# Kernel optimization log

Hardware: AMD Instinct MI355X
Metric: run time of the kernel (lower is better)

Reference implementation:

```python
import jax, jax.numpy as jnp
import numpy as np

TOP_K = 2  # matches init_kwargs top_k


def setup_inputs() -> dict:
    key = jax.random.key(0)
    ks = jax.random.split(key, 7)
    d_model, d_ff, E = 512, 2048, 8
    B, S = 2, 2048
    std = 0.02
    return {
        "x": jax.random.normal(ks[0], (B, S, d_model), dtype=jnp.float32),
        "Wr": jax.random.normal(ks[1], (E, d_model), dtype=jnp.float32) * std,
        "br": jnp.zeros((E,), dtype=jnp.float32),
        "W1": jax.random.normal(ks[2], (E, d_model, d_ff), dtype=jnp.float32) * (1.0 / np.sqrt(d_model)),
        "b1": jnp.zeros((E, d_ff), dtype=jnp.float32),
        "W2": jax.random.normal(ks[3], (E, d_ff, d_model), dtype=jnp.float32) * (1.0 / np.sqrt(d_ff)),
        "b2": jnp.zeros((E, d_model), dtype=jnp.float32),
    }


def _moe_forward(x, Wr, br, W1, b1, W2, b2):
    leading = x.shape[:-1]
    d = x.shape[-1]
    E = Wr.shape[0]
    xf = x.reshape(-1, d)                                   # [N, d]
    N = xf.shape[0]

    # --- token router (linear head) ---
    logits = xf @ Wr.T + br                                  # [N, E]
    routing = jax.nn.softmax(logits, axis=-1)                # [N, E]
    sel_w, sel_idx = jax.lax.top_k(routing, TOP_K)           # [N, K]
    sel_w = sel_w / jnp.sum(sel_w, axis=-1, keepdims=True)   # renormalize top-k

    # combine weights as dense [N, E] (zero for unselected experts)
    combine = jnp.zeros((N, E), dtype=xf.dtype).at[
        jnp.arange(N)[:, None], sel_idx
    ].add(sel_w)                                             # [N, E]

    # --- expert FFNs (dense all-expert compute, masked combine) ---
    h = jax.nn.gelu(jnp.einsum("nd,edf->enf", xf, W1) + b1[:, None, :])  # [E, N, ff]
    y = jnp.einsum("enf,efd->end", h, W2) + b2[:, None, :]               # [E, N, d]

    out = jnp.einsum("ne,end->nd", combine, y)               # [N, d]
    return out.reshape(*leading, d)


def reference(x, Wr, br, W1, b1, W2, b2):
    return _moe_forward(x, Wr, br, W1, b1, W2, b2)
```

## Files before the change

kernel.cpp:

```cpp
#include <hip/hip_runtime.h>
#include <hip/hip_bf16.h>
#include <cstdint>

typedef unsigned short u16;
typedef __bf16 bf16_t;
typedef __bf16 bf16x8 __attribute__((ext_vector_type(8)));
typedef float f32x4 __attribute__((ext_vector_type(4)));

#define DM   512
#define DFF  2048
#define NEXP 8

__device__ __forceinline__ u16 f2bf(float f) {
  bf16_t b = (bf16_t)f;
  return __builtin_bit_cast(u16, b);
}
__device__ __forceinline__ uint32_t pack_bf2(float lo, float hi) {
  return (uint32_t)f2bf(lo) | ((uint32_t)f2bf(hi) << 16);
}
__device__ __forceinline__ float gelu_tanh(float x) {
  float x3 = x * x * x;
  float z = 0.7978845608028654f * (x + 0.044715f * x3);
  float az = fabsf(z);
  float e = __expf(2.0f * az);
  float t = 1.0f - 2.0f / (e + 1.0f);
  t = copysignf(t, z);
  return 0.5f * x * (1.0f + t);
}
__device__ __forceinline__ void async16(const u16* g, u16* l) {
  __builtin_amdgcn_global_load_lds((const __attribute__((address_space(1))) void*)g,
                                   (__attribute__((address_space(3))) void*)l, 16, 0, 0);
}

__device__ __forceinline__ void transpose_tile(const float* __restrict__ s,
                                               u16* __restrict__ d, int R, int C,
                                               int tileIdx) {
  __shared__ u16 tile[64][66];
  int tilesC = C >> 6;
  int bR = (tileIdx / tilesC) << 6;
  int bC = (tileIdx % tilesC) << 6;
  int rr = threadIdx.x >> 4;
  int cc = (threadIdx.x & 15) << 2;
#pragma unroll
  for (int i = 0; i < 4; ++i) {
    int r = (i << 4) + rr;
    float4 v = *(const float4*)(s + (size_t)(bR + r) * C + bC + cc);
    *(uint32_t*)&tile[r][cc]     = pack_bf2(v.x, v.y);
    *(uint32_t*)&tile[r][cc + 2] = pack_bf2(v.z, v.w);
  }
  __syncthreads();
  int c0 = threadIdx.x >> 5;
  int j  = (threadIdx.x & 31) << 1;
#pragma unroll
  for (int i = 0; i < 8; ++i) {
    int c = (i << 3) + c0;
    uint32_t v = (uint32_t)tile[j][c] | ((uint32_t)tile[j + 1][c] << 16);
    *(uint32_t*)(&d[(size_t)(bC + c) * R + bR + j]) = v;
  }
}

__global__ void k_prep(const float* __restrict__ W1, u16* __restrict__ W1T,
                       const float* __restrict__ W2, u16* __restrict__ W2T,
                       const float* __restrict__ x, const float* __restrict__ Wr,
                       const float* __restrict__ br, int* __restrict__ sel_idx,
                       float* __restrict__ sel_w, int Ntok) {
  int b = blockIdx.x;
  if (b < 2048) {
    int e = b >> 8, t = b & 255;
    transpose_tile(W1 + (size_t)e * DM * DFF, W1T + (size_t)e * DM * DFF, DM, DFF, t);
    return;
  }
  if (b < 4096) {
    int e = (b - 2048) >> 8, t = (b - 2048) & 255;
    transpose_tile(W2 + (size_t)e * DFF * DM, W2T + (size_t)e * DFF * DM, DFF, DM, t);
    return;
  }
  int rb = b - 4096;
  int wid = threadIdx.x >> 6;
  int lane = threadIdx.x & 63;
  int tok = (rb << 2) + wid;
  if (tok >= Ntok) return;
  const float4* xr = (const float4*)(x + (size_t)tok * DM);
  float4 x0 = xr[lane * 2], x1 = xr[lane * 2 + 1];
  float logit[NEXP];
#pragma unroll
  for (int e = 0; e < NEXP; ++e) {
    const float4* wr = (const float4*)(Wr + e * DM);
    float4 w0 = wr[lane * 2], w1 = wr[lane * 2 + 1];
    float p = x0.x * w0.x + x0.y * w0.y + x0.z * w0.z + x0.w * w0.w
            + x1.x * w1.x + x1.y * w1.y + x1.z * w1.z + x1.w * w1.w;
#pragma unroll
    for (int off = 32; off; off >>= 1) p += __shfl_xor(p, off, 64);
    logit[e] = p + br[e];
  }
  if (lane == 0) {
    float mx = logit[0];
#pragma unroll
    for (int e = 1; e < NEXP; ++e) mx = fmaxf(mx, logit[e]);
    float pr[NEXP];
#pragma unroll
    for (int e = 0; e < NEXP; ++e) pr[e] = __expf(logit[e] - mx);
    int i0 = 0;
#pragma unroll
    for (int e = 1; e < NEXP; ++e) if (pr[e] > pr[i0]) i0 = e;
    int i1 = -1;
#pragma unroll
    for (int e = 0; e < NEXP; ++e) {
      if (e == i0) continue;
      if (i1 < 0 || pr[e] > pr[i1]) i1 = e;
    }
    float s2 = pr[i0] + pr[i1];
    sel_idx[tok * 2]     = i0;
    sel_idx[tok * 2 + 1] = i1;
    sel_w[tok * 2]       = pr[i0] / s2;
    sel_w[tok * 2 + 1]   = pr[i1] / s2;
  }
}

__global__ void k_scatter(const int* __restrict__ sel_idx, const float* __restrict__ sel_w,
                          int npairs, int* __restrict__ row_token, float* __restrict__ row_w,
                          int* __restrict__ pos_of, int* __restrict__ tileMeta,
                          int* __restrict__ gMeta) {
  __shared__ int cnt[NEXP], offs[NEXP], cur[NEXP];
  int tid = threadIdx.x;
  int lane = tid & 63;
  if (tid < NEXP) { cnt[tid] = 0; cur[tid] = 0; }
  __syncthreads();
  for (int p = tid; p < npairs; p += blockDim.x) {
    int e = sel_idx[p];
#pragma unroll
    for (int ex = 0; ex < NEXP; ++ex) {
      unsigned long long m = __ballot(e == ex);
      if (lane == 0 && m) atomicAdd(&cnt[ex], __popcll(m));
    }
  }
  __syncthreads();
  if (tid == 0) {
    int o = 0, nmt = 0;
    for (int e = 0; e < NEXP; ++e) {
      offs[e] = o;
      int c = cnt[e];
      int nt = (c + 127) >> 7;
      for (int t = 0; t < nt; ++t) {
        tileMeta[nmt * 3 + 0] = o + t * 128;
        tileMeta[nmt * 3 + 1] = o + c;
        tileMeta[nmt * 3 + 2] = e;
        ++nmt;
      }
      o += c;
    }
    gMeta[0] = nmt;
  }
  __syncthreads();
  for (int p = tid; p < npairs; p += blockDim.x) {
    int e = sel_idx[p];
    int pos = 0;
#pragma unroll
    for (int ex = 0; ex < NEXP; ++ex) {
      unsigned long long m = __ballot(e == ex);
      if (m) {
        int leader = __ffsll((long long)m) - 1;
        int base = 0;
        if (lane == leader) base = atomicAdd(&cur[ex], __popcll(m));
        base = __shfl(base, leader, 64);
        if (e == ex)
          pos = offs[ex] + base + __popcll(m & ((1ull << lane) - 1ull));
      }
    }
    row_token[pos] = p >> 1;
    row_w[pos] = sel_w[p];
    pos_of[p] = pos;
  }
}

__global__ void k_gather(const float* __restrict__ x, const int* __restrict__ row_token,
                         u16* __restrict__ Xg, int npairs) {
  int pos = (blockIdx.x << 2) + (threadIdx.x >> 6);
  int lane = threadIdx.x & 63;
  if (pos >= npairs) return;
  int tok = row_token[pos];
  const float4* src = (const float4*)(x + (size_t)tok * DM);
  float4 a = src[lane * 2], b = src[lane * 2 + 1];
  uint4 o;
  o.x = pack_bf2(a.x, a.y);
  o.y = pack_bf2(a.z, a.w);
  o.z = pack_bf2(b.x, b.y);
  o.w = pack_bf2(b.z, b.w);
  ((uint4*)(Xg + (size_t)pos * DM))[lane] = o;
}

template <int NFULL, int KTOT, int NSPLIT, bool GELU, bool SCALE>
__launch_bounds__(256)
__global__ void k_gemm(const u16* __restrict__ A, const u16* __restrict__ BT,
                       const float* __restrict__ bias, const float* __restrict__ row_w,
                       u16* __restrict__ Out, size_t pstride,
                       const int* __restrict__ tileMeta, const int* __restrict__ gMeta,
                       int maxmt) {
  constexpr int NTN = NFULL / 128;
  constexpr int SN  = (NTN >= 8) ? 8 : NTN;
  constexpr int NSN = NTN / SN;
  constexpr int SUPER = 8 * SN;
  constexpr int KCH = KTOT / NSPLIT;
  constexpr int NK  = KCH / 32;

  __shared__ __align__(16) u16 smem[24576];

  int NB = gridDim.x;
  int bid = blockIdx.x;
  int wg = ((NB & 7) == 0) ? ((bid & 7) * (NB >> 3) + (bid >> 3)) : bid;
  int s = wg / SUPER, l = wg % SUPER;
  int nsm = maxmt >> 3;
  int split = s / (nsm * NSN);
  int srem  = s % (nsm * NSN);
  int sm = srem / NSN, sn = srem % NSN;
  int mt = sm * 8 + l / SN;
  int nt = sn * SN + l % SN;
  if (mt >= gMeta[0]) return;
  int posStart = tileMeta[mt * 3 + 0];
  int segEnd   = tileMeta[mt * 3 + 1];
  int e        = tileMeta[mt * 3 + 2];

  int tid = threadIdx.x, lane = tid & 63, wid = tid >> 6;
  int wm = wid >> 1, wn = wid & 1;

  const u16* Ab = A + (size_t)split * KCH;
  const u16* Bb = BT + ((size_t)e * NFULL + (size_t)nt * 128) * KTOT + (size_t)split * KCH;

  int l4 = lane >> 2, c4 = lane & 3;
  const u16* aS[2];
  const u16* bS[2];
#pragma unroll
  for (int i = 0; i < 2; ++i) {
    int r = i * 64 + wid * 16 + l4;
    int g = posStart + r; if (g >= segEnd) g = segEnd - 1;
    int cs = c4 ^ ((r >> 1) & 3);
    aS[i] = Ab + (size_t)g * KTOT + cs * 8;
    bS[i] = Bb + (size_t)r * KTOT + cs * 8;
  }

  auto stage = [&](int kt, int slot) {
    u16* as = smem + slot * 8192;
    u16* bs = as + 4096;
#pragma unroll
    for (int i = 0; i < 2; ++i) {
      async16(aS[i] + kt * 32, as + i * 2048 + wid * 512);
      async16(bS[i] + kt * 32, bs + i * 2048 + wid * 512);
    }
  };

  f32x4 acc[4][4] = {};

  stage(0, 0);
  stage(1, 1);
  int bufC = 0, bufS = 2;
#pragma unroll 1
  for (int t = 0; t < NK; ++t) {
    if (t + 1 < NK) asm volatile("s_waitcnt vmcnt(4)" ::: "memory");
    else            asm volatile("s_waitcnt vmcnt(0)" ::: "memory");
    __builtin_amdgcn_s_barrier();
    asm volatile("" ::: "memory");
    if (t + 2 < NK) { stage(t + 2, bufS); bufS = (bufS == 2) ? 0 : bufS + 1; }
    const char* AsB = (const char*)(smem + bufC * 8192);
    const char* BsB = AsB + 8192;
    int kb = (lane >> 4) << 4;
    bf16x8 av[4], bv[4];
#pragma unroll
    for (int mi = 0; mi < 4; ++mi) {
      int row = (wm << 6) + (mi << 4) + (lane & 15);
      av[mi] = *(const bf16x8*)(AsB + row * 64 + (kb ^ (((row >> 1) & 3) << 4)));
    }
#pragma unroll
    for (int ni = 0; ni < 4; ++ni) {
      int row = (wn << 6) + (ni << 4) + (lane & 15);
      bv[ni] = *(const bf16x8*)(BsB + row * 64 + (kb ^ (((row >> 1) & 3) << 4)));
    }
    __builtin_amdgcn_s_setprio(1);
#pragma unroll
    for (int mi = 0; mi < 4; ++mi)
#pragma unroll
      for (int ni = 0; ni < 4; ++ni)
        acc[mi][ni] = __builtin_amdgcn_mfma_f32_16x16x32_bf16(av[mi], bv[ni], acc[mi][ni], 0, 0, 0);
    __builtin_amdgcn_s_setprio(0);
    bufC = (bufC == 2) ? 0 : bufC + 1;
  }

  __syncthreads();
  u16* Cs = smem;
  int laneCol = lane & 15;
  int laneRow4 = (lane >> 4) << 2;
  const float* biasE = bias + (size_t)e * NFULL;
  u16* OutS = Out + (size_t)split * pstride;
#pragma unroll
  for (int mi = 0; mi < 4; ++mi) {
#pragma unroll
    for (int j = 0; j < 4; ++j) {
      int r = (wm << 6) + (mi << 4) + laneRow4 + j;
      int m = posStart + r;
      int mc = m < segEnd ? m : segEnd - 1;
      float w = 1.0f;
      if constexpr (SCALE) w = row_w[mc];
#pragma unroll
      for (int ni = 0; ni < 4; ++ni) {
        int cl = (wn << 6) + (ni << 4) + laneCol;
        float v = acc[mi][ni][j];
        if (split == 0) v += biasE[nt * 128 + cl];
        if constexpr (GELU) v = gelu_tanh(v);
        if constexpr (SCALE) v *= w;
        Cs[r * 136 + cl] = f2bf(v);
      }
    }
  }
  __syncthreads();
  int r0 = tid >> 4, q = tid & 15;
#pragma unroll
  for (int i = 0; i < 8; ++i) {
    int r = (i << 4) + r0;
    if (posStart + r < segEnd)
      *((uint4*)(OutS + (size_t)(posStart + r) * NFULL + (nt << 7)) + q) =
          ((uint4*)(Cs + (size_t)r * 136))[q];
  }
}

template <int NSPLIT>
__global__ void k_combine(const u16* __restrict__ P, size_t pstride,
                          const int* __restrict__ pos_of, float* __restrict__ out, int Ntok) {
  int tok = (blockIdx.x << 2) + (threadIdx.x >> 6);
  int lane = threadIdx.x & 63;
  if (tok >= Ntok) return;
  int p0 = pos_of[tok * 2], p1 = pos_of[tok * 2 + 1];
  float s[8] = {};
#pragma unroll
  for (int sp = 0; sp < NSPLIT; ++sp) {
    bf16x8 a = ((const bf16x8*)(P + sp * pstride + (size_t)p0 * DM))[lane];
    bf16x8 b = ((const bf16x8*)(P + sp * pstride + (size_t)p1 * DM))[lane];
#pragma unroll
    for (int i = 0; i < 8; ++i) s[i] += (float)a[i] + (float)b[i];
  }
  float4* o = (float4*)(out + (size_t)tok * DM + lane * 8);
  o[0] = make_float4(s[0], s[1], s[2], s[3]);
  o[1] = make_float4(s[4], s[5], s[6], s[7]);
}

extern "C" void kernel_launch(void* const* d_in, const int* in_sizes, int n_in,
                              void* d_out, int out_size, void* d_ws, size_t ws_size,
                              hipStream_t stream) {
  const float* x  = (const float*)d_in[0];
  const float* Wr = (const float*)d_in[1];
  const float* br = (const float*)d_in[2];
  const float* W1 = (const float*)d_in[3];
  const float* b1 = (const float*)d_in[4];
  const float* W2 = (const float*)d_in[5];
  const float* b2 = (const float*)d_in[6];
  float* out = (float*)d_out;

  int Ntok = in_sizes[0] / DM;
  int npairs = Ntok * 2;
  int maxmt = npairs / 128 + NEXP;
  size_t pstride = (size_t)npairs * DM;

  char* p = (char*)d_ws;
  u16* W1T = (u16*)p;  p += (size_t)NEXP * DFF * DM * 2;
  u16* W2T = (u16*)p;  p += (size_t)NEXP * DM * DFF * 2;
  u16* Xg  = (u16*)p;  p += (size_t)npairs * DM * 2;
  u16* H   = (u16*)p;  p += (size_t)npairs * DFF * 2;
  u16* Part = (u16*)p; p += 2 * pstride * 2;
  int* sel_idx   = (int*)p;   p += (size_t)npairs * 4;
  float* sel_w   = (float*)p; p += (size_t)npairs * 4;
  int* pos_of    = (int*)p;   p += (size_t)npairs * 4;
  int* row_token = (int*)p;   p += (size_t)npairs * 4;
  float* row_w   = (float*)p; p += (size_t)npairs * 4;
  int* tileMeta  = (int*)p;   p += (size_t)(maxmt * 3 + 16) * 4;
  int* gMeta     = (int*)p;   p += 64;

  k_prep<<<dim3(4096 + Ntok / 4), 256, 0, stream>>>(W1, W1T, W2, W2T, x, Wr, br,
                                                    sel_idx, sel_w, Ntok);
  k_scatter<<<dim3(1), 1024, 0, stream>>>(sel_idx, sel_w, npairs, row_token, row_w,
                                          pos_of, tileMeta, gMeta);
  k_gather<<<dim3(npairs / 4), 256, 0, stream>>>(x, row_token, Xg, npairs);
  k_gemm<DFF, DM, 1, true, false>
      <<<dim3(maxmt * (DFF / 128)), 256, 0, stream>>>(
          Xg, W1T, b1, nullptr, H, 0, tileMeta, gMeta, maxmt);
  k_gemm<DM, DFF, 2, false, true>
      <<<dim3(maxmt * (DM / 128) * 2), 256, 0, stream>>>(
          H, W2T, b2, row_w, Part, pstride, tileMeta, gMeta, maxmt);
  k_combine<2><<<dim3(Ntok / 4), 256, 0, stream>>>(Part, pstride, pos_of, out, Ntok);
}
```

Baseline: 143.3 us.

## Shrink GEMM LDS to double buffer and split epilogue into two halves

```diff
diff --git a/kernel.cpp b/kernel.cpp
--- a/kernel.cpp
+++ b/kernel.cpp
@@ -203,7 +203,7 @@
   constexpr int KCH = KTOT / NSPLIT;
   constexpr int NK  = KCH / 32;
 
-  __shared__ __align__(16) u16 smem[24576];
+  __shared__ __align__(16) u16 smem[16384];
 
   int NB = gridDim.x;
   int bid = blockIdx.x;
@@ -251,16 +251,14 @@
   f32x4 acc[4][4] = {};
 
   stage(0, 0);
-  stage(1, 1);
-  int bufC = 0, bufS = 2;
+  asm volatile("s_waitcnt vmcnt(0)" ::: "memory");
+  __builtin_amdgcn_s_barrier();
+  asm volatile("" ::: "memory");
+
 #pragma unroll 1
   for (int t = 0; t < NK; ++t) {
-    if (t + 1 < NK) asm volatile("s_waitcnt vmcnt(4)" ::: "memory");
-    else            asm volatile("s_waitcnt vmcnt(0)" ::: "memory");
-    __builtin_amdgcn_s_barrier();
-    asm volatile("" ::: "memory");
-    if (t + 2 < NK) { stage(t + 2, bufS); bufS = (bufS == 2) ? 0 : bufS + 1; }
-    const char* AsB = (const char*)(smem + bufC * 8192);
+    if (t + 1 < NK) stage(t + 1, (t + 1) & 1);
+    const char* AsB = (const char*)(smem + (t & 1) * 8192);
     const char* BsB = AsB + 8192;
     int kb = (lane >> 4) << 4;
     bf16x8 av[4], bv[4];
@@ -281,43 +279,51 @@
       for (int ni = 0; ni < 4; ++ni)
         acc[mi][ni] = __builtin_amdgcn_mfma_f32_16x16x32_bf16(av[mi], bv[ni], acc[mi][ni], 0, 0, 0);
     __builtin_amdgcn_s_setprio(0);
-    bufC = (bufC == 2) ? 0 : bufC + 1;
-  }
-
-  __syncthreads();
+    if (t + 1 < NK) asm volatile("s_waitcnt vmcnt(0)" ::: "memory");
+    __builtin_amdgcn_s_barrier();
+    asm volatile("" ::: "memory");
+  }
+
   u16* Cs = smem;
+  const float* biasE = bias + (size_t)e * NFULL;
+  u16* OutS = Out + (size_t)split * pstride;
   int laneCol = lane & 15;
   int laneRow4 = (lane >> 4) << 2;
-  const float* biasE = bias + (size_t)e * NFULL;
-  u16* OutS = Out + (size_t)split * pstride;
-#pragma unroll
-  for (int mi = 0; mi < 4; ++mi) {
-#pragma unroll
-    for (int j = 0; j < 4; ++j) {
-      int r = (wm << 6) + (mi << 4) + laneRow4 + j;
-      int m = posStart + r;
-      int mc = m < segEnd ? m : segEnd - 1;
-      float w = 1.0f;
-      if constexpr (SCALE) w = row_w[mc];
-#pragma unroll
-      for (int ni = 0; ni < 4; ++ni) {
-        int cl = (wn << 6) + (ni << 4) + laneCol;
-        float v = acc[mi][ni][j];
-        if (split == 0) v += biasE[nt * 128 + cl];
-        if constexpr (GELU) v = gelu_tanh(v);
-        if constexpr (SCALE) v *= w;
-        Cs[r * 136 + cl] = f2bf(v);
+#pragma unroll
+  for (int ch = 0; ch < 2; ++ch) {
+    __syncthreads();
+    if (wm == ch) {
+#pragma unroll
+      for (int mi = 0; mi < 4; ++mi) {
+#pragma unroll
+        for (int j = 0; j < 4; ++j) {
+          int rl = (mi << 4) + laneRow4 + j;
+          int m = posStart + (ch << 6) + rl;
+          int mc = m < segEnd ? m : segEnd - 1;
+          float w = 1.0f;
+          if constexpr (SCALE) w = row_w[mc];
+#pragma unroll
+          for (int ni = 0; ni < 4; ++ni) {
+            int cl = (wn << 6) + (ni << 4) + laneCol;
+            float v = acc[mi][ni][j];
+            if (split == 0) v += biasE[nt * 128 + cl];
+            if constexpr (GELU) v = gelu_tanh(v);
+            if constexpr (SCALE) v *= w;
+            Cs[rl * 136 + cl] = f2bf(v);
+          }
+        }
       }
     }
-  }
-  __syncthreads();
-  int r0 = tid >> 4, q = tid & 15;
-#pragma unroll
-  for (int i = 0; i < 8; ++i) {
-    int r = (i << 4) + r0;
-    if (posStart + r < segEnd)
-      *((uint4*)(OutS + (size_t)(posStart + r) * NFULL + (nt << 7)) + q) =
-          ((uint4*)(Cs + (size_t)r * 136))[q];
+    __syncthreads();
+    int r0 = tid >> 4, q = tid & 15;
+#pragma unroll
+    for (int i = 0; i < 4; ++i) {
+      int rl = (i << 4) + r0;
+      int m = posStart + (ch << 6) + rl;
+      if (m < segEnd)
+        *((uint4*)(OutS + (size_t)m * NFULL + (nt << 7)) + q) =
+            ((uint4*)(Cs + (size_t)rl * 136))[q];
+    }
   }
 }
 
```

Measured after the change: 165.5 us. +15.5%, slower.
